# Kernel optimization log

Measured on AMD Instinct MI355X. Metric: run time of the kernel, lower is better.

The kernel has to match this reference:

```python
import jax, jax.numpy as jnp
import numpy as np

B, S, D_MODEL, D_QK = 4, 4096, 256, 64


def setup_inputs() -> dict:
    key = jax.random.key(0)
    ks = jax.random.split(key, 6)
    enc_q = jax.random.normal(ks[0], (B, S, D_MODEL), dtype=jnp.float32)
    enc_k = jax.random.normal(ks[1], (B, S, D_MODEL), dtype=jnp.float32)
    enc_v = jax.random.normal(ks[2], (B, S, D_MODEL), dtype=jnp.float32)
    # torch nn.Linear weight layout: [out_features, in_features]
    Wq = jax.random.normal(ks[3], (D_QK, D_MODEL), dtype=jnp.float32) * (D_MODEL ** -0.5)
    Wk = jax.random.normal(ks[4], (D_QK, D_MODEL), dtype=jnp.float32) * (D_MODEL ** -0.5)
    Wv = jax.random.normal(ks[5], (D_MODEL, D_MODEL), dtype=jnp.float32) * (D_MODEL ** -0.5)
    # causal mask: True above the diagonal -> masked out (matches masked_fill semantics)
    mask = jnp.triu(jnp.ones((S, S), dtype=jnp.bool_), k=1)
    return {"encodings_for_q": enc_q, "encodings_for_k": enc_k,
            "encodings_for_v": enc_v, "mask": mask,
            "Wq": Wq, "Wk": Wk, "Wv": Wv}


def reference(encodings_for_q, encodings_for_k, encodings_for_v, mask, Wq, Wk, Wv):
    # linear projections (no bias): x @ W.T
    q = jnp.einsum('bsd,qd->bsq', encodings_for_q, Wq)   # [B,S,d_qk]
    k = jnp.einsum('bsd,qd->bsq', encodings_for_k, Wk)   # [B,S,d_qk]
    v = jnp.einsum('bsd,ed->bse', encodings_for_v, Wv)   # [B,S,d_model]
    scale = k.shape[-1] ** 0.5                            # sqrt(d_qk)
    sims = jnp.einsum('bsq,btq->bst', q, k) / scale       # [B,S,S]
    sims = jnp.where(mask, jnp.float32(-1e9), sims)
    attn = jax.nn.softmax(sims, axis=-1)
    return jnp.einsum('bst,bte->bse', attn, v)            # [B,S,d_model]
```

## Files before the change

### kernel.cpp

```cpp
#include <hip/hip_runtime.h>


#define BATCH 4
#define SEQ   4096
#define DM    256
#define DQK   64

typedef __bf16 bf16x8 __attribute__((ext_vector_type(8)));
typedef float  f32x16 __attribute__((ext_vector_type(16)));

__device__ __forceinline__ unsigned int rnd16(unsigned int u) {
    return u + 0x7fffu + ((u >> 16) & 1u);
}
__device__ __forceinline__ unsigned short f2bf(float f) {
    return (unsigned short)(rnd16(__builtin_bit_cast(unsigned int, f)) >> 16);
}
__device__ __forceinline__ unsigned int pk2bf(float lo, float hi) {
    unsigned int a = rnd16(__builtin_bit_cast(unsigned int, lo));
    unsigned int b = rnd16(__builtin_bit_cast(unsigned int, hi));
    return (a >> 16) | (b & 0xffff0000u);
}
__device__ __forceinline__ bf16x8 u4bf(uint4 u) { return __builtin_bit_cast(bf16x8, u); }

__device__ __forceinline__ void repack_store(const f32x16& acc, int q2, int l,
                                             uint4* __restrict__ out, size_t tile_ofs_u4) {
    unsigned int d0[4], d1[4], p0[4], p1[4];
#pragma unroll
    for (int h = 0; h < 4; ++h) {
        d0[h] = pk2bf(acc[4*h + 0], acc[4*h + 1]);
        d1[h] = pk2bf(acc[4*h + 2], acc[4*h + 3]);
        p0[h] = __shfl_xor((int)d0[h], 32);
        p1[h] = __shfl_xor((int)d1[h], 32);
    }
#pragma unroll
    for (int kc = 0; kc < 2; ++kc) {
        int h = 2*kc + q2;
        uint4 v = (q2 == 0) ? make_uint4(d0[h], d1[h], p0[h], p1[h])
                            : make_uint4(p0[h], p1[h], d0[h], d1[h]);
        out[tile_ofs_u4 + (size_t)kc * 64 + l] = v;
    }
}

__device__ __forceinline__ int obase(int T) {
    return (T < 24) ? (T - 12) : 12 + (T - 24) * 2;
}
__device__ __forceinline__ int dbase(int T) {
    return (T < 24) ? (T - 12) * 2 : 24 + (T - 24) * 3;
}

__global__ __launch_bounds__(256) void proj(const float* __restrict__ Xq,
                                            const float* __restrict__ Xk,
                                            const float* __restrict__ Xv,
                                            const float* __restrict__ Wq,
                                            const float* __restrict__ Wk,
                                            const float* __restrict__ Wv,
                                            uint4* __restrict__ qf,
                                            uint4* __restrict__ kf,
                                            uint4* __restrict__ vf) {
    __shared__ unsigned short Xs[64][264];
    __shared__ unsigned short Ws[64][264];

    const int z = blockIdx.z;
    const int bx = blockIdx.x, b = blockIdx.y;
    const float* X = (z == 0) ? Xq : (z == 1) ? Xk : Xv;
    const float* W = (z == 0) ? Wq : (z == 1) ? Wk : Wv;
    const int s0 = bx * 64;
    const int tid = threadIdx.x, w = tid >> 6, l = tid & 63, ln = l & 31, q2 = l >> 5;

#pragma unroll
    for (int i = 0; i < 16; ++i) {
        int f = i * 256 + tid;
        int r = f >> 6, c4 = f & 63;
        float4 xv = *(const float4*)&X[((size_t)b * SEQ + s0 + r) * DM + c4 * 4];
        ushort4 h; h.x = f2bf(xv.x); h.y = f2bf(xv.y); h.z = f2bf(xv.z); h.w = f2bf(xv.w);
        *(ushort4*)&Xs[r][c4 * 4] = h;
    }

    if (z < 2) {
#pragma unroll
        for (int i = 0; i < 16; ++i) {
            int f = i * 256 + tid;
            int r = f >> 6, c4 = f & 63;
            float4 wv = *(const float4*)&W[(size_t)r * DM + c4 * 4];
            ushort4 h; h.x = f2bf(wv.x); h.y = f2bf(wv.y); h.z = f2bf(wv.z); h.w = f2bf(wv.w);
            *(ushort4*)&Ws[r][c4 * 4] = h;
        }
        __syncthreads();
        const int msub = w >> 1, nsub = w & 1;
        f32x16 a0 = {}, a1 = {};
#pragma unroll
        for (int c = 0; c < 16; c += 2) {
            bf16x8 af0 = u4bf(*(const uint4*)&Ws[msub*32 + ln][c*16 + q2*8]);
            bf16x8 bf0 = u4bf(*(const uint4*)&Xs[nsub*32 + ln][c*16 + q2*8]);
            a0 = __builtin_amdgcn_mfma_f32_32x32x16_bf16(af0, bf0, a0, 0, 0, 0);
            bf16x8 af1 = u4bf(*(const uint4*)&Ws[msub*32 + ln][(c+1)*16 + q2*8]);
            bf16x8 bf1 = u4bf(*(const uint4*)&Xs[nsub*32 + ln][(c+1)*16 + q2*8]);
            a1 = __builtin_amdgcn_mfma_f32_32x32x16_bf16(af1, bf1, a1, 0, 0, 0);
        }
        f32x16 acc = a0 + a1;
        size_t base = (((size_t)(b*128 + bx*2 + nsub)) * 4 + 2*msub) * 64;
        repack_store(acc, q2, l, (z == 0) ? qf : kf, base);
    } else {
        const int msub = w & 1, nsub = w >> 1;
        for (int ecl = 0; ecl < 2; ++ecl) {
            const int ec = (z - 2) * 2 + ecl;
            __syncthreads();
#pragma unroll
            for (int i = 0; i < 16; ++i) {
                int f = i * 256 + tid;
                int r = f >> 6, c4 = f & 63;
                float4 wv = *(const float4*)&W[(size_t)(ec*64 + r) * DM + c4 * 4];
                ushort4 h; h.x = f2bf(wv.x); h.y = f2bf(wv.y); h.z = f2bf(wv.z); h.w = f2bf(wv.w);
                *(ushort4*)&Ws[r][c4 * 4] = h;
            }
            __syncthreads();
            f32x16 a0 = {}, a1 = {};
#pragma unroll
            for (int c = 0; c < 16; c += 2) {
                bf16x8 af0 = u4bf(*(const uint4*)&Xs[msub*32 + ln][c*16 + q2*8]);
                bf16x8 bf0 = u4bf(*(const uint4*)&Ws[nsub*32 + ln][c*16 + q2*8]);
                a0 = __builtin_amdgcn_mfma_f32_32x32x16_bf16(af0, bf0, a0, 0, 0, 0);
                bf16x8 af1 = u4bf(*(const uint4*)&Xs[msub*32 + ln][(c+1)*16 + q2*8]);
                bf16x8 bf1 = u4bf(*(const uint4*)&Ws[nsub*32 + ln][(c+1)*16 + q2*8]);
                a1 = __builtin_amdgcn_mfma_f32_32x32x16_bf16(af1, bf1, a1, 0, 0, 0);
            }
            f32x16 acc = a0 + a1;
            int et = ec*2 + nsub;
            size_t base = (((size_t)(b*8 + et)) * 256 + (size_t)bx*4 + msub*2) * 64;
            repack_store(acc, q2, l, vf, base);
        }
    }
}

__global__ __launch_bounds__(512, 4) void attn(const uint4* __restrict__ qf,
                                               const uint4* __restrict__ kf,
                                               const uint4* __restrict__ vf,
                                               float* __restrict__ out,
                                               unsigned short* __restrict__ Op,
                                               float* __restrict__ Dp) {
    __shared__ uint4 Pb[2][4][8][64];
    __shared__ float denp[8][2][64];
    __shared__ float dfin[128];

    const int bid = blockIdx.x;
    const int eh = bid >> 8, r_ = bid & 255;
    const int slot = r_ & 7, u = r_ >> 3;
    const int b = slot >> 1;
    const int task = u * 2 + (slot & 1);
    if (task >= 60) return;
    int T, cc, nc;
    if (task < 12)      { T = task;                cc = 0;               nc = 1; }
    else if (task < 36) { int q = task - 12; T = 12 + (q >> 1); cc = q & 1;       nc = 2; }
    else                { int q = task - 36; T = 24 + q / 3;    cc = q - 3*(q/3); nc = 3; }
    const int n = T + 1;
    const int j0 = cc * n / nc, j1 = (cc + 1) * n / nc;

    const int tid = threadIdx.x, w = tid >> 6, l = tid & 63, ln = l & 31, q2 = l >> 5;
    const int ks = w & 3, qp = w >> 2;
    const int etl = w & 3, qh = w >> 2;
    const int et = eh * 4 + etl;
    const float cfac = 0.18033688011112042f;

    bf16x8 qv[2][4];
#pragma unroll
    for (int g = 0; g < 2; ++g)
#pragma unroll
        for (int c = 0; c < 4; ++c)
            qv[g][c] = u4bf(qf[(((size_t)b*128 + T*4 + qp*2 + g) * 4 + c) * 64 + l]);

    f32x16 oa[2] = {};
    float den[2] = {0.f, 0.f};

    uint4 kaf[4];
#pragma unroll
    for (int c = 0; c < 4; ++c)
        kaf[c] = kf[(((size_t)b*128 + j0*4 + ks) * 4 + c) * 64 + l];

    for (int jt = j0; jt < j1; ++jt) {
        const int buf = jt & 1;
        const bool diag = (jt == T);
        f32x16 s0 = {}, s1 = {};
#pragma unroll
        for (int c = 0; c < 4; ++c) {
            bf16x8 ka = u4bf(kaf[c]);
            s0 = __builtin_amdgcn_mfma_f32_32x32x16_bf16(ka, qv[0][c], s0, 0, 0, 0);
            s1 = __builtin_amdgcn_mfma_f32_32x32x16_bf16(ka, qv[1][c], s1, 0, 0, 0);
        }
#pragma unroll
        for (int g = 0; g < 2; ++g) {
            const f32x16 s = g ? s1 : s0;
            const int qsub = qp*2 + g;
            float pv[16], pd = 0.f;
#pragma unroll
            for (int r = 0; r < 16; ++r) {
                float e = __builtin_exp2f(s[r] * cfac);
                if (diag) {
                    int klocal = 4*q2 + (r & 3) + 8*(r >> 2);
                    if (ks*32 + klocal > qsub*32 + ln) e = 0.f;
                }
                pv[r] = e; pd += e;
            }
            den[g] += pd;
#pragma unroll
            for (int quad = 0; quad < 4; ++quad) {
                unsigned int lo = pk2bf(pv[4*quad + 0], pv[4*quad + 1]);
                unsigned int hi = pk2bf(pv[4*quad + 2], pv[4*quad + 3]);
                int kcg = ks*2 + (quad >> 1);
                int h   = quad & 1;
                char* dst = (char*)&Pb[buf][qsub][kcg][h*32 + ln] + q2*8;
                *(uint2*)dst = make_uint2(lo, hi);
            }
        }
        __syncthreads();
        if (jt + 1 < j1) {
#pragma unroll
            for (int c = 0; c < 4; ++c)
                kaf[c] = kf[(((size_t)b*128 + (jt+1)*4 + ks) * 4 + c) * 64 + l];
        }
        uint4 vbs[8];
#pragma unroll
        for (int kc = 0; kc < 8; ++kc)
            vbs[kc] = vf[(((size_t)b*8 + et) * 256 + (size_t)jt*8 + kc) * 64 + l];
#pragma unroll
        for (int kc = 0; kc < 8; ++kc) {
            bf16x8 vb = u4bf(vbs[kc]);
            bf16x8 pa0 = u4bf(Pb[buf][qh*2 + 0][kc][l]);
            oa[0] = __builtin_amdgcn_mfma_f32_32x32x16_bf16(pa0, vb, oa[0], 0, 0, 0);
            bf16x8 pa1 = u4bf(Pb[buf][qh*2 + 1][kc][l]);
            oa[1] = __builtin_amdgcn_mfma_f32_32x32x16_bf16(pa1, vb, oa[1], 0, 0, 0);
        }
    }

    denp[w][0][l] = den[0];
    denp[w][1][l] = den[1];
    __syncthreads();
    if (tid < 128) {
        int qsub = tid >> 5, qln = tid & 31;
        int g = qsub & 1, wp = qsub >> 1;
        float sden = 0.f;
#pragma unroll
        for (int k4 = 0; k4 < 4; ++k4)
#pragma unroll
            for (int hh = 0; hh < 2; ++hh)
                sden += denp[wp*4 + k4][g][hh*32 + qln];
        dfin[tid] = (nc == 1) ? 1.0f / sden : sden;
    }
    __syncthreads();

    const int col = et*32 + ln;
    if (nc == 1) {
#pragma unroll
        for (int j = 0; j < 2; ++j)
#pragma unroll
            for (int r = 0; r < 16; ++r) {
                int qrow = (qh*2 + j)*32 + (r & 3) + 8*(r >> 2) + 4*q2;
                out[((size_t)b*SEQ + T*128 + qrow) * DM + col] = oa[j][r] * dfin[qrow];
            }
    } else if (cc == 0) {
#pragma unroll
        for (int j = 0; j < 2; ++j)
#pragma unroll
            for (int r = 0; r < 16; ++r) {
                int qrow = (qh*2 + j)*32 + (r & 3) + 8*(r >> 2) + 4*q2;
                out[((size_t)b*SEQ + T*128 + qrow) * DM + col] = oa[j][r];
            }
        if (eh == 0 && tid < 128) Dp[((size_t)b*48 + dbase(T)) * 128 + tid] = dfin[tid];
    } else {
        size_t pidx = (size_t)b*28 + obase(T) + (cc - 1);
#pragma unroll
        for (int j = 0; j < 2; ++j)
#pragma unroll
            for (int r = 0; r < 16; ++r) {
                int qrow = (qh*2 + j)*32 + (r & 3) + 8*(r >> 2) + 4*q2;
                Op[(pidx*128 + qrow) * DM + col] = f2bf(oa[j][r]);
            }
        if (eh == 0 && tid < 128) Dp[((size_t)b*48 + dbase(T) + cc) * 128 + tid] = dfin[tid];
    }
}

__global__ __launch_bounds__(256) void combine(const unsigned short* __restrict__ Op,
                                               const float* __restrict__ Dp,
                                               float* __restrict__ out) {
    const int T = 12 + blockIdx.x, b = blockIdx.y, qq = blockIdx.z;
    const int nc = (T < 24) ? 2 : 3;
    const int t = threadIdx.x;
    const size_t db = (size_t)b*48 + dbase(T);
    const size_t pb = (size_t)b*28 + obase(T);
#pragma unroll 4
    for (int r = 0; r < 32; ++r) {
        int q = qq*32 + r;
        size_t oofs = ((size_t)b*SEQ + T*128 + q) * DM + t;
        float sum = out[oofs];
        float dsum = 0.f;
        for (int c = 0; c < nc; ++c) dsum += Dp[(db + c)*128 + q];
        for (int c = 1; c < nc; ++c) {
            unsigned int uv = Op[((pb + c - 1)*128 + q) * DM + t];
            sum += __builtin_bit_cast(float, uv << 16);
        }
        out[oofs] = sum / dsum;
    }
}

extern "C" void kernel_launch(void* const* d_in, const int* in_sizes, int n_in,
                              void* d_out, int out_size, void* d_ws, size_t ws_size,
                              hipStream_t stream) {
    const float* enc_q = (const float*)d_in[0];
    const float* enc_k = (const float*)d_in[1];
    const float* enc_v = (const float*)d_in[2];
    const float* Wq = (const float*)d_in[4];
    const float* Wk = (const float*)d_in[5];
    const float* Wv = (const float*)d_in[6];
    float* out = (float*)d_out;

    uint4* qf = (uint4*)d_ws;
    uint4* kf = qf + 131072;
    uint4* vf = kf + 131072;
    unsigned short* Op = (unsigned short*)(vf + 524288);
    float* Dp = (float*)(Op + (size_t)4*28*128*256);

    proj<<<dim3(64, 4, 4), 256, 0, stream>>>(enc_q, enc_k, enc_v, Wq, Wk, Wv, qf, kf, vf);
    attn<<<512, 512, 0, stream>>>(qf, kf, vf, out, Op, Dp);
    combine<<<dim3(20, 4, 4), 256, 0, stream>>>(Op, Dp, out);
}
```

Measured before the change: 225.6 us.

## Merge the two value-column halves into one attention block per task

Before, each query tile/chunk task ran as two blocks, one per half of the 256 value columns, and each block recomputed QK^T scores and the softmax probabilities. Now one block computes all 256 output columns: each of the 8 waves owns a 32-column slice and accumulates four query subtiles, the grid shrinks from 512 to 240 blocks, and the launch-bounds occupancy hint drops from 4 to 2. The V tile loads also move ahead of the score MFMAs so they overlap with the softmax. This removes the duplicated score and exp work, at the cost of twice the accumulator registers per thread, lower occupancy, and fewer blocks to spread across the compute units.

```diff
diff --git a/kernel.cpp b/kernel.cpp
--- a/kernel.cpp
+++ b/kernel.cpp
@@ -132,7 +132,7 @@
     }
 }
 
-__global__ __launch_bounds__(512, 4) void attn(const uint4* __restrict__ qf,
+__global__ __launch_bounds__(512, 2) void attn(const uint4* __restrict__ qf,
                                                const uint4* __restrict__ kf,
                                                const uint4* __restrict__ vf,
                                                float* __restrict__ out,
@@ -143,11 +143,9 @@
     __shared__ float dfin[128];
 
     const int bid = blockIdx.x;
-    const int eh = bid >> 8, r_ = bid & 255;
-    const int slot = r_ & 7, u = r_ >> 3;
+    const int slot = bid & 7, u = bid >> 3;
     const int b = slot >> 1;
     const int task = u * 2 + (slot & 1);
-    if (task >= 60) return;
     int T, cc, nc;
     if (task < 12)      { T = task;                cc = 0;               nc = 1; }
     else if (task < 36) { int q = task - 12; T = 12 + (q >> 1); cc = q & 1;       nc = 2; }
@@ -157,8 +155,6 @@
 
     const int tid = threadIdx.x, w = tid >> 6, l = tid & 63, ln = l & 31, q2 = l >> 5;
     const int ks = w & 3, qp = w >> 2;
-    const int etl = w & 3, qh = w >> 2;
-    const int et = eh * 4 + etl;
     const float cfac = 0.18033688011112042f;
 
     bf16x8 qv[2][4];
@@ -168,7 +164,7 @@
         for (int c = 0; c < 4; ++c)
             qv[g][c] = u4bf(qf[(((size_t)b*128 + T*4 + qp*2 + g) * 4 + c) * 64 + l]);
 
-    f32x16 oa[2] = {};
+    f32x16 oa[4] = {};
     float den[2] = {0.f, 0.f};
 
     uint4 kaf[4];
@@ -179,6 +175,12 @@
     for (int jt = j0; jt < j1; ++jt) {
         const int buf = jt & 1;
         const bool diag = (jt == T);
+
+        uint4 vbs[8];
+#pragma unroll
+        for (int kc = 0; kc < 8; ++kc)
+            vbs[kc] = vf[(((size_t)b*8 + w) * 256 + (size_t)jt*8 + kc) * 64 + l];
+
         f32x16 s0 = {}, s1 = {};
 #pragma unroll
         for (int c = 0; c < 4; ++c) {
@@ -217,17 +219,14 @@
             for (int c = 0; c < 4; ++c)
                 kaf[c] = kf[(((size_t)b*128 + (jt+1)*4 + ks) * 4 + c) * 64 + l];
         }
-        uint4 vbs[8];
-#pragma unroll
-        for (int kc = 0; kc < 8; ++kc)
-            vbs[kc] = vf[(((size_t)b*8 + et) * 256 + (size_t)jt*8 + kc) * 64 + l];
 #pragma unroll
         for (int kc = 0; kc < 8; ++kc) {
             bf16x8 vb = u4bf(vbs[kc]);
-            bf16x8 pa0 = u4bf(Pb[buf][qh*2 + 0][kc][l]);
-            oa[0] = __builtin_amdgcn_mfma_f32_32x32x16_bf16(pa0, vb, oa[0], 0, 0, 0);
-            bf16x8 pa1 = u4bf(Pb[buf][qh*2 + 1][kc][l]);
-            oa[1] = __builtin_amdgcn_mfma_f32_32x32x16_bf16(pa1, vb, oa[1], 0, 0, 0);
+#pragma unroll
+            for (int qs = 0; qs < 4; ++qs) {
+                bf16x8 pa = u4bf(Pb[buf][qs][kc][l]);
+                oa[qs] = __builtin_amdgcn_mfma_f32_32x32x16_bf16(pa, vb, oa[qs], 0, 0, 0);
+            }
         }
     }
 
@@ -247,34 +246,33 @@
     }
     __syncthreads();
 
-    const int col = et*32 + ln;
     if (nc == 1) {
 #pragma unroll
-        for (int j = 0; j < 2; ++j)
+        for (int qs = 0; qs < 4; ++qs)
 #pragma unroll
             for (int r = 0; r < 16; ++r) {
-                int qrow = (qh*2 + j)*32 + (r & 3) + 8*(r >> 2) + 4*q2;
-                out[((size_t)b*SEQ + T*128 + qrow) * DM + col] = oa[j][r] * dfin[qrow];
+                int qrow = qs*32 + (r & 3) + 8*(r >> 2) + 4*q2;
+                out[((size_t)b*SEQ + T*128 + qrow) * DM + w*32 + ln] = oa[qs][r] * dfin[qrow];
             }
     } else if (cc == 0) {
 #pragma unroll
-        for (int j = 0; j < 2; ++j)
+        for (int qs = 0; qs < 4; ++qs)
 #pragma unroll
             for (int r = 0; r < 16; ++r) {
-                int qrow = (qh*2 + j)*32 + (r & 3) + 8*(r >> 2) + 4*q2;
-                out[((size_t)b*SEQ + T*128 + qrow) * DM + col] = oa[j][r];
-            }
-        if (eh == 0 && tid < 128) Dp[((size_t)b*48 + dbase(T)) * 128 + tid] = dfin[tid];
+                int qrow = qs*32 + (r & 3) + 8*(r >> 2) + 4*q2;
+                out[((size_t)b*SEQ + T*128 + qrow) * DM + w*32 + ln] = oa[qs][r];
+            }
+        if (tid < 128) Dp[((size_t)b*48 + dbase(T)) * 128 + tid] = dfin[tid];
     } else {
         size_t pidx = (size_t)b*28 + obase(T) + (cc - 1);
 #pragma unroll
-        for (int j = 0; j < 2; ++j)
+        for (int qs = 0; qs < 4; ++qs)
 #pragma unroll
             for (int r = 0; r < 16; ++r) {
-                int qrow = (qh*2 + j)*32 + (r & 3) + 8*(r >> 2) + 4*q2;
-                Op[(pidx*128 + qrow) * DM + col] = f2bf(oa[j][r]);
-            }
-        if (eh == 0 && tid < 128) Dp[((size_t)b*48 + dbase(T) + cc) * 128 + tid] = dfin[tid];
+                int qrow = qs*32 + (r & 3) + 8*(r >> 2) + 4*q2;
+                Op[(pidx*128 + qrow) * DM + w*32 + ln] = f2bf(oa[qs][r]);
+            }
+        if (tid < 128) Dp[((size_t)b*48 + dbase(T) + cc) * 128 + tid] = dfin[tid];
     }
 }
 
@@ -319,6 +317,6 @@
     float* Dp = (float*)(Op + (size_t)4*28*128*256);
 
     proj<<<dim3(64, 4, 4), 256, 0, stream>>>(enc_q, enc_k, enc_v, Wq, Wk, Wv, qf, kf, vf);
-    attn<<<512, 512, 0, stream>>>(qf, kf, vf, out, Op, Dp);
+    attn<<<240, 512, 0, stream>>>(qf, kf, vf, out, Op, Dp);
     combine<<<dim3(20, 4, 4), 256, 0, stream>>>(Op, Dp, out);
 }
```

Result: faster. 206.7 us (-8.4%).
